# Kernel optimization log

Measured on AMD Instinct MI355X. Metric: run time of the kernel, lower is better.

## Reference

```python
import jax, jax.numpy as jnp
import numpy as np

N = 100000   # nodes
E = 1600000  # edges (avg degree 16)
D = 128      # in = hidden = out channels
DROP_P = 0.2


def setup_inputs() -> dict:
    key = jax.random.key(0)
    ks = jax.random.split(key, 11)
    s = 1.0 / np.sqrt(D)  # glorot-ish scale
    inp = {
        "features": jax.random.normal(ks[0], (N, D), jnp.float32),
        "edge_index": jax.random.randint(ks[1], (2, E), 0, N, dtype=jnp.int64),
    }
    for i in range(3):
        inp[f"Wl{i}"] = jax.random.normal(ks[2 + 3 * i], (D, D), jnp.float32) * s
        inp[f"Wr{i}"] = jax.random.normal(ks[3 + 3 * i], (D, D), jnp.float32) * s
        inp[f"b{i}"] = jnp.zeros((D,), jnp.float32)
    return inp


def _sage_conv(x, src, dst, Wl, Wr, b):
    # PyG SAGEConv (aggr='max'): out = lin_l(max_{j->i} x_j) + lin_r(x_i)
    agg = jax.ops.segment_max(x[src], dst, num_segments=N)  # [N, D_in]
    agg = jnp.where(jnp.isfinite(agg), agg, 0.0)  # isolated nodes -> 0 (torch_scatter zero-init)
    return agg @ Wl + x @ Wr + b


def _dropout(x, key, p=DROP_P):
    keep = jax.random.bernoulli(key, 1.0 - p, x.shape)
    return jnp.where(keep, x / (1.0 - p), 0.0)


def reference(features, edge_index, Wl0, Wr0, b0, Wl1, Wr1, b1, Wl2, Wr2, b2):
    src, dst = edge_index[0], edge_index[1]
    k1, k2 = jax.random.split(jax.random.key(42))
    x = _sage_conv(features, src, dst, Wl0, Wr0, b0)
    x = _dropout(jax.nn.elu(x), k1)
    x = _sage_conv(x, src, dst, Wl1, Wr1, b1)
    x = _dropout(jax.nn.elu(x), k2)
    x = _sage_conv(x, src, dst, Wl2, Wr2, b2)
    return x
```

## Files before the change

kernel.cpp:

```cpp
#include <hip/hip_runtime.h>
#include <math.h>

#define D 128
#define CHUNK 1024
#define BSHIFT 9
#define BCAP 12288

typedef __attribute__((ext_vector_type(8))) _Float16 half8;
typedef __attribute__((ext_vector_type(4))) float floatx4;

__host__ __device__ __forceinline__ unsigned rotl32(unsigned v, int r) {
  return (v << r) | (v >> (32 - r));
}

__host__ __device__ __forceinline__ void threefry2x32(unsigned k0, unsigned k1,
                                                      unsigned x0, unsigned x1,
                                                      unsigned &o0, unsigned &o1) {
  unsigned ks2 = k0 ^ k1 ^ 0x1BD11BDAu;
  unsigned v0 = x0 + k0;
  unsigned v1 = x1 + k1;
  v0 += v1; v1 = rotl32(v1, 13); v1 ^= v0;
  v0 += v1; v1 = rotl32(v1, 15); v1 ^= v0;
  v0 += v1; v1 = rotl32(v1, 26); v1 ^= v0;
  v0 += v1; v1 = rotl32(v1, 6);  v1 ^= v0;
  v0 += k1; v1 += ks2 + 1u;
  v0 += v1; v1 = rotl32(v1, 17); v1 ^= v0;
  v0 += v1; v1 = rotl32(v1, 29); v1 ^= v0;
  v0 += v1; v1 = rotl32(v1, 16); v1 ^= v0;
  v0 += v1; v1 = rotl32(v1, 24); v1 ^= v0;
  v0 += ks2; v1 += k0 + 2u;
  v0 += v1; v1 = rotl32(v1, 13); v1 ^= v0;
  v0 += v1; v1 = rotl32(v1, 15); v1 ^= v0;
  v0 += v1; v1 = rotl32(v1, 26); v1 ^= v0;
  v0 += v1; v1 = rotl32(v1, 6);  v1 ^= v0;
  v0 += k0; v1 += k1 + 3u;
  v0 += v1; v1 = rotl32(v1, 17); v1 ^= v0;
  v0 += v1; v1 = rotl32(v1, 29); v1 ^= v0;
  v0 += v1; v1 = rotl32(v1, 16); v1 ^= v0;
  v0 += v1; v1 = rotl32(v1, 24); v1 ^= v0;
  v0 += k1; v1 += ks2 + 4u;
  v0 += v1; v1 = rotl32(v1, 13); v1 ^= v0;
  v0 += v1; v1 = rotl32(v1, 15); v1 ^= v0;
  v0 += v1; v1 = rotl32(v1, 26); v1 ^= v0;
  v0 += v1; v1 = rotl32(v1, 6);  v1 ^= v0;
  v0 += ks2; v1 += k0 + 5u;
  o0 = v0; o1 = v1;
}

__device__ __forceinline__ unsigned short f2h(float f) {
  _Float16 h = (_Float16)f;
  return *(unsigned short*)&h;
}

__device__ __forceinline__ unsigned pkmax(unsigned a, unsigned b) {
  unsigned r;
  asm("v_pk_max_f16 %0, %1, %2" : "=v"(r) : "v"(a), "v"(b));
  return r;
}

__global__ __launch_bounds__(256) void hist_kernel(
    const int* __restrict__ dst, int* __restrict__ counts, int nEdges) {
  int e = blockIdx.x * 256 + threadIdx.x;
  if (e < nEdges) atomicAdd(&counts[dst[e]], 1);
}

__global__ __launch_bounds__(256) void reduce_chunk_kernel(
    const int* __restrict__ counts, int* __restrict__ blockSums, int nNodes) {
  __shared__ int s[256];
  int t = threadIdx.x;
  int base = blockIdx.x * CHUNK + t * 4;
  int sum = 0;
#pragma unroll
  for (int i = 0; i < 4; ++i)
    if (base + i < nNodes) sum += counts[base + i];
  s[t] = sum;
  __syncthreads();
  for (int off = 128; off > 0; off >>= 1) {
    if (t < off) s[t] += s[t + off];
    __syncthreads();
  }
  if (t == 0) blockSums[blockIdx.x] = s[0];
}

__global__ void scan_block_sums_kernel(int* blockSums, int nChunks) {
  if (threadIdx.x == 0 && blockIdx.x == 0) {
    int run = 0;
    for (int i = 0; i < nChunks; ++i) {
      int v = blockSums[i];
      blockSums[i] = run;
      run += v;
    }
    blockSums[nChunks] = run;
  }
}

__global__ __launch_bounds__(256) void scan_chunk_kernel(
    const int* __restrict__ counts, const int* __restrict__ blockOffs,
    int* __restrict__ rowStart, int* __restrict__ cursor, int nNodes) {
  __shared__ int sSum[256];
  int t = threadIdx.x;
  int base = blockIdx.x * CHUNK + t * 4;
  int c0 = 0, c1 = 0, c2 = 0, c3 = 0;
  if (base + 0 < nNodes) c0 = counts[base + 0];
  if (base + 1 < nNodes) c1 = counts[base + 1];
  if (base + 2 < nNodes) c2 = counts[base + 2];
  if (base + 3 < nNodes) c3 = counts[base + 3];
  int local = c0 + c1 + c2 + c3;
  sSum[t] = local;
  __syncthreads();
  for (int off = 1; off < 256; off <<= 1) {
    int v = (t >= off) ? sSum[t - off] : 0;
    __syncthreads();
    sSum[t] += v;
    __syncthreads();
  }
  int excl = blockOffs[blockIdx.x] + sSum[t] - local;
  int p0 = excl, p1 = p0 + c0, p2 = p1 + c1, p3 = p2 + c2;
  if (base + 0 < nNodes) { rowStart[base + 0] = p0; cursor[base + 0] = p0;
                           if (base + 0 == nNodes - 1) rowStart[nNodes] = p1; }
  if (base + 1 < nNodes) { rowStart[base + 1] = p1; cursor[base + 1] = p1;
                           if (base + 1 == nNodes - 1) rowStart[nNodes] = p2; }
  if (base + 2 < nNodes) { rowStart[base + 2] = p2; cursor[base + 2] = p2;
                           if (base + 2 == nNodes - 1) rowStart[nNodes] = p3; }
  if (base + 3 < nNodes) { rowStart[base + 3] = p3; cursor[base + 3] = p3;
                           if (base + 3 == nNodes - 1) rowStart[nNodes] = p3 + c3; }
}

__global__ void init_bucket_cursor_kernel(
    const int* __restrict__ rowStart, int* __restrict__ bucketCursor,
    int nBuck, int nNodes) {
  int b = blockIdx.x * 256 + threadIdx.x;
  if (b <= nBuck) {
    int n = b << BSHIFT;
    if (n > nNodes) n = nNodes;
    bucketCursor[b] = rowStart[n];
  }
}

__global__ __launch_bounds__(256) void bucket_scatter_kernel(
    const int* __restrict__ src, const int* __restrict__ dst,
    int* __restrict__ bucketCursor, uint2* __restrict__ pairs,
    int nEdges, int nBuck) {
  __shared__ int lcount[256];
  __shared__ int lbase[256];
  __shared__ int loff[256];
  int t = threadIdx.x;
  lcount[t] = 0; loff[t] = 0;
  __syncthreads();
  int e0 = blockIdx.x * 4096;
  for (int i = t; i < 4096; i += 256) {
    int e = e0 + i;
    if (e < nEdges) atomicAdd(&lcount[dst[e] >> BSHIFT], 1);
  }
  __syncthreads();
  if (t < nBuck) {
    int c = lcount[t];
    if (c > 0) lbase[t] = atomicAdd(&bucketCursor[t], c);
  }
  __syncthreads();
  for (int i = t; i < 4096; i += 256) {
    int e = e0 + i;
    if (e < nEdges) {
      int d = dst[e];
      int b = d >> BSHIFT;
      int lp = atomicAdd(&loff[b], 1);
      pairs[lbase[b] + lp] = make_uint2((unsigned)src[e], (unsigned)d);
    }
  }
}

__global__ __launch_bounds__(256) void local_fill_kernel(
    const uint2* __restrict__ pairs, const int* __restrict__ rowStart,
    int* __restrict__ cursor, int* __restrict__ csrSrc, int nNodes) {
  __shared__ int sData[BCAP];
  __shared__ int lcur[1 << BSHIFT];
  int b = blockIdx.x;
  int node0 = b << BSHIFT;
  int node1 = node0 + (1 << BSHIFT);
  if (node1 > nNodes) node1 = nNodes;
  int base = rowStart[node0];
  int end = rowStart[node1];
  int cnt = end - base;
  int t = threadIdx.x;
  for (int i = t; i < node1 - node0; i += 256)
    lcur[i] = rowStart[node0 + i] - base;
  __syncthreads();
  if (cnt <= BCAP) {
    for (int i = base + t; i < end; i += 256) {
      uint2 p = pairs[i];
      int lp = atomicAdd(&lcur[p.y - (unsigned)node0], 1);
      sData[lp] = (int)p.x;
    }
    __syncthreads();
    for (int i = t; i < cnt; i += 256)
      csrSrc[base + i] = sData[i];
  } else {
    for (int i = base + t; i < end; i += 256) {
      uint2 p = pairs[i];
      int pos = atomicAdd(&cursor[p.y], 1);
      csrSrc[pos] = (int)p.x;
    }
  }
}

__global__ __launch_bounds__(256) void convert_feat_kernel(
    const float* __restrict__ f, unsigned short* __restrict__ o, int nElems) {
  int i = (blockIdx.x * 256 + threadIdx.x) * 4;
  if (i + 3 < nElems) {
    float4 v = *((const float4*)(f + i));
    unsigned a = (unsigned)f2h(v.x) | ((unsigned)f2h(v.y) << 16);
    unsigned b = (unsigned)f2h(v.z) | ((unsigned)f2h(v.w) << 16);
    *((uint2*)(o + i)) = make_uint2(a, b);
  } else {
    for (int j = i; j < nElems; ++j) o[j] = f2h(f[j]);
  }
}

__global__ __launch_bounds__(256) void pack_weights_kernel(
    const float* __restrict__ Wl0, const float* __restrict__ Wr0,
    const float* __restrict__ Wl1, const float* __restrict__ Wr1,
    const float* __restrict__ Wl2, const float* __restrict__ Wr2,
    unsigned short* __restrict__ Wt) {
  int t = blockIdx.x * 256 + threadIdx.x;
  if (t >= 3 * 128 * 256) return;
  int l = t >> 15;
  int rem = t & 32767;
  int n = rem >> 8;
  int k = rem & 255;
  const float* Wl = (l == 0) ? Wl0 : (l == 1) ? Wl1 : Wl2;
  const float* Wr = (l == 0) ? Wr0 : (l == 1) ? Wr1 : Wr2;
  float v = (k < 128) ? Wl[k * D + n] : Wr[(k - 128) * D + n];
  Wt[t] = f2h(v);
}

__global__ __launch_bounds__(256) void gather_max_f16_kernel(
    const uint4* __restrict__ x8, const int* __restrict__ rowStart,
    const int* __restrict__ csrSrc, uint4* __restrict__ agg8, int nNodes) {
  int n = blockIdx.x * 4 + (threadIdx.x >> 6);
  if (n >= nNodes) return;
  int lane = threadIdx.x & 63;
  int q = lane >> 4;
  int l16 = lane & 15;
  int e0 = rowStart[n], e1 = rowStart[n + 1];
  unsigned m0 = 0xFC00FC00u, m1 = 0xFC00FC00u,
           m2 = 0xFC00FC00u, m3 = 0xFC00FC00u;
  int e = e0;
  for (; e + 7 < e1; e += 8) {
    int sa = csrSrc[e + q];
    int sb = csrSrc[e + 4 + q];
    uint4 va = x8[(size_t)sa * 16 + l16];
    uint4 vb = x8[(size_t)sb * 16 + l16];
    m0 = pkmax(m0, pkmax(va.x, vb.x));
    m1 = pkmax(m1, pkmax(va.y, vb.y));
    m2 = pkmax(m2, pkmax(va.z, vb.z));
    m3 = pkmax(m3, pkmax(va.w, vb.w));
  }
  if (e + 3 < e1) {
    int sa = csrSrc[e + q];
    uint4 va = x8[(size_t)sa * 16 + l16];
    m0 = pkmax(m0, va.x); m1 = pkmax(m1, va.y);
    m2 = pkmax(m2, va.z); m3 = pkmax(m3, va.w);
    e += 4;
  }
  for (; e < e1; ++e) {
    int sa = csrSrc[e];
    uint4 va = x8[(size_t)sa * 16 + l16];
    m0 = pkmax(m0, va.x); m1 = pkmax(m1, va.y);
    m2 = pkmax(m2, va.z); m3 = pkmax(m3, va.w);
  }
  m0 = pkmax(m0, (unsigned)__shfl_xor((int)m0, 16, 64));
  m1 = pkmax(m1, (unsigned)__shfl_xor((int)m1, 16, 64));
  m2 = pkmax(m2, (unsigned)__shfl_xor((int)m2, 16, 64));
  m3 = pkmax(m3, (unsigned)__shfl_xor((int)m3, 16, 64));
  m0 = pkmax(m0, (unsigned)__shfl_xor((int)m0, 32, 64));
  m1 = pkmax(m1, (unsigned)__shfl_xor((int)m1, 32, 64));
  m2 = pkmax(m2, (unsigned)__shfl_xor((int)m2, 32, 64));
  m3 = pkmax(m3, (unsigned)__shfl_xor((int)m3, 32, 64));
  uint4 r = make_uint4(0u, 0u, 0u, 0u);
  if (e0 != e1) r = make_uint4(m0, m1, m2, m3);
  if (q == 0) agg8[(size_t)n * 16 + l16] = r;
}

#define PA 280

__global__ __launch_bounds__(256) void fused_mfma_kernel(
    const unsigned short* __restrict__ agghf, unsigned short* __restrict__ xhf,
    const unsigned short* __restrict__ Wt, const float* __restrict__ bias,
    float* __restrict__ outF, int nRows, int mode, unsigned kk0, unsigned kk1) {
  __shared__ unsigned short sA[32 * PA];

  const int tid = threadIdx.x;
  const int row0 = blockIdx.x * 32;
  const int wv = tid >> 6, lane = tid & 63;
  const int quad = lane >> 4, m16 = lane & 15;
  const int nbase = wv * 32;

#pragma unroll
  for (int i = 0; i < 4; ++i) {
    int idx = i * 256 + tid;
    int r = idx >> 5;
    int seg = idx & 31;
    uint4 v = make_uint4(0, 0, 0, 0);
    if (row0 + r < nRows) {
      if (seg < 16) v = ((const uint4*)(agghf + (size_t)(row0 + r) * D))[seg];
      else          v = ((const uint4*)(xhf  + (size_t)(row0 + r) * D))[seg - 16];
    }
    *((uint4*)(sA + r * PA + seg * 8)) = v;
  }

  half8 bfr[2][4][2];
#pragma unroll
  for (int kc = 0; kc < 2; ++kc)
#pragma unroll
    for (int ks = 0; ks < 4; ++ks)
#pragma unroll
      for (int j = 0; j < 2; ++j)
        bfr[kc][ks][j] = *((const half8*)(
            Wt + (size_t)(nbase + j * 16 + m16) * 256 + kc * 128 + ks * 32 + quad * 8));

  floatx4 acc[2][2];
#pragma unroll
  for (int i = 0; i < 2; ++i)
#pragma unroll
    for (int j = 0; j < 2; ++j) acc[i][j] = (floatx4)(0.0f);

  __syncthreads();

#pragma unroll
  for (int kc = 0; kc < 2; ++kc)
#pragma unroll
    for (int ks = 0; ks < 4; ++ks) {
      int kA = kc * 128 + ks * 32 + quad * 8;
      half8 a0 = *((const half8*)(sA + m16 * PA + kA));
      half8 a1 = *((const half8*)(sA + (m16 + 16) * PA + kA));
      acc[0][0] = __builtin_amdgcn_mfma_f32_16x16x32_f16(a0, bfr[kc][ks][0], acc[0][0], 0, 0, 0);
      acc[0][1] = __builtin_amdgcn_mfma_f32_16x16x32_f16(a0, bfr[kc][ks][1], acc[0][1], 0, 0, 0);
      acc[1][0] = __builtin_amdgcn_mfma_f32_16x16x32_f16(a1, bfr[kc][ks][0], acc[1][0], 0, 0, 0);
      acc[1][1] = __builtin_amdgcn_mfma_f32_16x16x32_f16(a1, bfr[kc][ks][1], acc[1][1], 0, 0, 0);
    }

#pragma unroll
  for (int j = 0; j < 2; ++j) {
    int col = nbase + j * 16 + m16;
    float bc = bias[col];
#pragma unroll
    for (int i = 0; i < 2; ++i) {
#pragma unroll
      for (int reg = 0; reg < 4; ++reg) {
        int r = row0 + i * 16 + quad * 4 + reg;
        if (r >= nRows) continue;
        float v = acc[i][j][reg] + bc;
        if (mode < 2) {
          v = (v > 0.0f) ? v : expm1f(v);
          unsigned jj = (unsigned)r * D + col;
          unsigned y0, y1;
          threefry2x32(kk0, kk1, 0u, jj, y0, y1);
          float u = __uint_as_float((((y0 ^ y1) >> 9)) | 0x3F800000u) - 1.0f;
          v = (u < 0.8f) ? v * 1.25f : 0.0f;
          xhf[(size_t)r * D + col] = f2h(v);
        } else {
          outF[(size_t)r * D + col] = v;
        }
      }
    }
  }
}

extern "C" void kernel_launch(void* const* d_in, const int* in_sizes, int n_in,
                              void* d_out, int out_size, void* d_ws, size_t ws_size,
                              hipStream_t stream) {
  const float* feat = (const float*)d_in[0];
  const int* ei = (const int*)d_in[1];
  const float* Wl0 = (const float*)d_in[2];
  const float* Wr0 = (const float*)d_in[3];
  const float* b0 = (const float*)d_in[4];
  const float* Wl1 = (const float*)d_in[5];
  const float* Wr1 = (const float*)d_in[6];
  const float* b1 = (const float*)d_in[7];
  const float* Wl2 = (const float*)d_in[8];
  const float* Wr2 = (const float*)d_in[9];
  const float* b2 = (const float*)d_in[10];

  const int N = in_sizes[0] / D;
  const int E = in_sizes[1] / 2;
  const int* src = ei;
  const int* dst = ei + E;

  const size_t hfBytes = (size_t)N * D * 2;
  char* wsp = (char*)d_ws;
  size_t off = 0;
  unsigned short* xhf   = (unsigned short*)(wsp + off); off += hfBytes;
  unsigned short* agghf = (unsigned short*)(wsp + off); off += hfBytes;
  unsigned short* Wt    = (unsigned short*)(wsp + off); off += ((size_t)3 * 128 * 256 * 2 + 511) & ~511ull;
  int* rowStart  = (int*)(wsp + off); off += ((size_t)(N + 1) * 4 + 511) & ~511ull;
  int* cursor    = (int*)(wsp + off); off += ((size_t)N * 4 + 511) & ~511ull;
  int* blockSums = (int*)(wsp + off); off += 2048;
  int* bucketCursor = (int*)(wsp + off); off += 4096;
  int* csrSrc    = (int*)(wsp + off); off += (size_t)E * 4;
  uint2* pairs   = (uint2*)(wsp + off); off += (size_t)E * 8;

  const int nChunks = (N + CHUNK - 1) / CHUNK;
  const int nBuck = (N + (1 << BSHIFT) - 1) >> BSHIFT;

  unsigned k1a, k1b, k2a, k2b;
  threefry2x32(0u, 42u, 0u, 0u, k1a, k1b);
  threefry2x32(0u, 42u, 0u, 1u, k2a, k2b);

  hipMemsetAsync(cursor, 0, (size_t)N * 4, stream);
  hist_kernel<<<(E + 255) / 256, 256, 0, stream>>>(dst, cursor, E);
  reduce_chunk_kernel<<<nChunks, 256, 0, stream>>>(cursor, blockSums, N);
  scan_block_sums_kernel<<<1, 64, 0, stream>>>(blockSums, nChunks);
  scan_chunk_kernel<<<nChunks, 256, 0, stream>>>(cursor, blockSums, rowStart, cursor, N);
  init_bucket_cursor_kernel<<<(nBuck + 256) / 256, 256, 0, stream>>>(rowStart, bucketCursor, nBuck, N);
  bucket_scatter_kernel<<<(E + 4095) / 4096, 256, 0, stream>>>(src, dst, bucketCursor, pairs, E, nBuck);
  local_fill_kernel<<<nBuck, 256, 0, stream>>>(pairs, rowStart, cursor, csrSrc, N);

  convert_feat_kernel<<<(N * D / 4 + 255) / 256, 256, 0, stream>>>(feat, xhf, N * D);
  pack_weights_kernel<<<(3 * 128 * 256 + 255) / 256, 256, 0, stream>>>(
      Wl0, Wr0, Wl1, Wr1, Wl2, Wr2, Wt);

  dim3 blk(256);
  dim3 grdMax((N + 3) / 4);
  dim3 grdGemm((N + 31) / 32);
  float* outF = (float*)d_out;

  gather_max_f16_kernel<<<grdMax, blk, 0, stream>>>((const uint4*)xhf, rowStart, csrSrc, (uint4*)agghf, N);
  fused_mfma_kernel<<<grdGemm, blk, 0, stream>>>(agghf, xhf, Wt, b0, outF, N, 0, k1a, k1b);

  gather_max_f16_kernel<<<grdMax, blk, 0, stream>>>((const uint4*)xhf, rowStart, csrSrc, (uint4*)agghf, N);
  fused_mfma_kernel<<<grdGemm, blk, 0, stream>>>(agghf, xhf, Wt + 32768, b1, outF, N, 1, k2a, k2b);

  gather_max_f16_kernel<<<grdMax, blk, 0, stream>>>((const uint4*)xhf, rowStart, csrSrc, (uint4*)agghf, N);
  fused_mfma_kernel<<<grdGemm, blk, 0, stream>>>(agghf, xhf, Wt + 65536, b2, outF, N, 2, 0u, 0u);
}
```

Before: 588.9 us.

## Build CSR via bucket-level counts and pack edge pairs into one word

Replaces the per-node global histogram and the multi-kernel prefix scan with a per-bucket count, a single-block bucket scan, and a per-node count and scan done in shared memory inside local_fill_kernel, which also writes rowStart. Edge pairs are packed into 32 bits (source shifted left by 9 bits, low 9 bits of the destination) instead of uint2, halving the scratch traffic. This removes several launches and the global atomics on 100k counters. The packing only works while source ids fit in 23 bits and there are at most 256 buckets.

```diff
diff --git a/kernel.cpp b/kernel.cpp
--- a/kernel.cpp
+++ b/kernel.cpp
@@ -2,7 +2,6 @@
 #include <math.h>
 
 #define D 128
-#define CHUNK 1024
 #define BSHIFT 9
 #define BCAP 12288
 
@@ -58,88 +57,49 @@
   return r;
 }
 
-__global__ __launch_bounds__(256) void hist_kernel(
-    const int* __restrict__ dst, int* __restrict__ counts, int nEdges) {
-  int e = blockIdx.x * 256 + threadIdx.x;
-  if (e < nEdges) atomicAdd(&counts[dst[e]], 1);
-}
-
-__global__ __launch_bounds__(256) void reduce_chunk_kernel(
-    const int* __restrict__ counts, int* __restrict__ blockSums, int nNodes) {
+
+__global__ __launch_bounds__(256) void bucket_count_kernel(
+    const int* __restrict__ dst, int* __restrict__ bucketTotal, int nEdges) {
+  __shared__ int lc[256];
+  int t = threadIdx.x;
+  lc[t] = 0;
+  __syncthreads();
+  int e0 = blockIdx.x * 4096;
+  for (int i = t; i < 4096; i += 256) {
+    int e = e0 + i;
+    if (e < nEdges) atomicAdd(&lc[dst[e] >> BSHIFT], 1);
+  }
+  __syncthreads();
+  int c = lc[t];
+  if (c > 0) atomicAdd(&bucketTotal[t], c);
+}
+
+__global__ __launch_bounds__(256) void scan_buckets_kernel(
+    const int* __restrict__ bucketTotal, int* __restrict__ buckOff,
+    int* __restrict__ bucketCursor, int nBuck) {
   __shared__ int s[256];
   int t = threadIdx.x;
-  int base = blockIdx.x * CHUNK + t * 4;
-  int sum = 0;
-#pragma unroll
-  for (int i = 0; i < 4; ++i)
-    if (base + i < nNodes) sum += counts[base + i];
-  s[t] = sum;
-  __syncthreads();
-  for (int off = 128; off > 0; off >>= 1) {
-    if (t < off) s[t] += s[t + off];
+  int v = (t < nBuck) ? bucketTotal[t] : 0;
+  s[t] = v;
+  __syncthreads();
+  for (int off = 1; off < 256; off <<= 1) {
+    int u = (t >= off) ? s[t - off] : 0;
     __syncthreads();
-  }
-  if (t == 0) blockSums[blockIdx.x] = s[0];
-}
-
-__global__ void scan_block_sums_kernel(int* blockSums, int nChunks) {
-  if (threadIdx.x == 0 && blockIdx.x == 0) {
-    int run = 0;
-    for (int i = 0; i < nChunks; ++i) {
-      int v = blockSums[i];
-      blockSums[i] = run;
-      run += v;
-    }
-    blockSums[nChunks] = run;
-  }
-}
-
-__global__ __launch_bounds__(256) void scan_chunk_kernel(
-    const int* __restrict__ counts, const int* __restrict__ blockOffs,
-    int* __restrict__ rowStart, int* __restrict__ cursor, int nNodes) {
-  __shared__ int sSum[256];
-  int t = threadIdx.x;
-  int base = blockIdx.x * CHUNK + t * 4;
-  int c0 = 0, c1 = 0, c2 = 0, c3 = 0;
-  if (base + 0 < nNodes) c0 = counts[base + 0];
-  if (base + 1 < nNodes) c1 = counts[base + 1];
-  if (base + 2 < nNodes) c2 = counts[base + 2];
-  if (base + 3 < nNodes) c3 = counts[base + 3];
-  int local = c0 + c1 + c2 + c3;
-  sSum[t] = local;
-  __syncthreads();
-  for (int off = 1; off < 256; off <<= 1) {
-    int v = (t >= off) ? sSum[t - off] : 0;
+    s[t] += u;
     __syncthreads();
-    sSum[t] += v;
-    __syncthreads();
-  }
-  int excl = blockOffs[blockIdx.x] + sSum[t] - local;
-  int p0 = excl, p1 = p0 + c0, p2 = p1 + c1, p3 = p2 + c2;
-  if (base + 0 < nNodes) { rowStart[base + 0] = p0; cursor[base + 0] = p0;
-                           if (base + 0 == nNodes - 1) rowStart[nNodes] = p1; }
-  if (base + 1 < nNodes) { rowStart[base + 1] = p1; cursor[base + 1] = p1;
-                           if (base + 1 == nNodes - 1) rowStart[nNodes] = p2; }
-  if (base + 2 < nNodes) { rowStart[base + 2] = p2; cursor[base + 2] = p2;
-                           if (base + 2 == nNodes - 1) rowStart[nNodes] = p3; }
-  if (base + 3 < nNodes) { rowStart[base + 3] = p3; cursor[base + 3] = p3;
-                           if (base + 3 == nNodes - 1) rowStart[nNodes] = p3 + c3; }
-}
-
-__global__ void init_bucket_cursor_kernel(
-    const int* __restrict__ rowStart, int* __restrict__ bucketCursor,
-    int nBuck, int nNodes) {
-  int b = blockIdx.x * 256 + threadIdx.x;
-  if (b <= nBuck) {
-    int n = b << BSHIFT;
-    if (n > nNodes) n = nNodes;
-    bucketCursor[b] = rowStart[n];
+  }
+  int excl = s[t] - v;
+  if (t < nBuck) {
+    buckOff[t] = excl;
+    bucketCursor[t] = excl;
+  } else if (t == nBuck) {
+    buckOff[t] = s[255];
   }
 }
 
 __global__ __launch_bounds__(256) void bucket_scatter_kernel(
     const int* __restrict__ src, const int* __restrict__ dst,
-    int* __restrict__ bucketCursor, uint2* __restrict__ pairs,
+    int* __restrict__ bucketCursor, unsigned* __restrict__ pairs,
     int nEdges, int nBuck) {
   __shared__ int lcount[256];
   __shared__ int lbase[256];
@@ -164,41 +124,69 @@
       int d = dst[e];
       int b = d >> BSHIFT;
       int lp = atomicAdd(&loff[b], 1);
-      pairs[lbase[b] + lp] = make_uint2((unsigned)src[e], (unsigned)d);
+      pairs[lbase[b] + lp] = ((unsigned)src[e] << BSHIFT) | ((unsigned)d & 511u);
     }
   }
 }
 
 __global__ __launch_bounds__(256) void local_fill_kernel(
-    const uint2* __restrict__ pairs, const int* __restrict__ rowStart,
-    int* __restrict__ cursor, int* __restrict__ csrSrc, int nNodes) {
+    const unsigned* __restrict__ pairs, const int* __restrict__ buckOff,
+    int* __restrict__ rowStart, int* __restrict__ csrSrc,
+    int nNodes, int nBuck) {
   __shared__ int sData[BCAP];
-  __shared__ int lcur[1 << BSHIFT];
+  __shared__ int lcnt[1 << BSHIFT];
+  __shared__ int sSum[256];
   int b = blockIdx.x;
   int node0 = b << BSHIFT;
-  int node1 = node0 + (1 << BSHIFT);
-  if (node1 > nNodes) node1 = nNodes;
-  int base = rowStart[node0];
-  int end = rowStart[node1];
+  int base = buckOff[b];
+  int end = buckOff[b + 1];
   int cnt = end - base;
   int t = threadIdx.x;
-  for (int i = t; i < node1 - node0; i += 256)
-    lcur[i] = rowStart[node0 + i] - base;
-  __syncthreads();
+
+  lcnt[t] = 0;
+  lcnt[t + 256] = 0;
+  __syncthreads();
+
+  for (int i = base + t; i < end; i += 256)
+    atomicAdd(&lcnt[pairs[i] & 511u], 1);
+  __syncthreads();
+
+  int c0 = lcnt[2 * t];
+  int c1 = lcnt[2 * t + 1];
+  int local = c0 + c1;
+  sSum[t] = local;
+  __syncthreads();
+  for (int off = 1; off < 256; off <<= 1) {
+    int v = (t >= off) ? sSum[t - off] : 0;
+    __syncthreads();
+    sSum[t] += v;
+    __syncthreads();
+  }
+  int excl = sSum[t] - local;
+  __syncthreads();
+  lcnt[2 * t] = excl;
+  lcnt[2 * t + 1] = excl + c0;
+  int n0 = node0 + 2 * t;
+  int n1 = n0 + 1;
+  if (n0 < nNodes) rowStart[n0] = base + excl;
+  if (n1 < nNodes) rowStart[n1] = base + excl + c0;
+  if (b == nBuck - 1 && t == 255) rowStart[nNodes] = end;
+  __syncthreads();
+
   if (cnt <= BCAP) {
     for (int i = base + t; i < end; i += 256) {
-      uint2 p = pairs[i];
-      int lp = atomicAdd(&lcur[p.y - (unsigned)node0], 1);
-      sData[lp] = (int)p.x;
+      unsigned p = pairs[i];
+      int lp = atomicAdd(&lcnt[p & 511u], 1);
+      sData[lp] = (int)(p >> BSHIFT);
     }
     __syncthreads();
     for (int i = t; i < cnt; i += 256)
       csrSrc[base + i] = sData[i];
   } else {
     for (int i = base + t; i < end; i += 256) {
-      uint2 p = pairs[i];
-      int pos = atomicAdd(&cursor[p.y], 1);
-      csrSrc[pos] = (int)p.x;
+      unsigned p = pairs[i];
+      int lp = atomicAdd(&lcnt[p & 511u], 1);
+      csrSrc[base + lp] = (int)(p >> BSHIFT);
     }
   }
 }
@@ -392,28 +380,24 @@
   unsigned short* xhf   = (unsigned short*)(wsp + off); off += hfBytes;
   unsigned short* agghf = (unsigned short*)(wsp + off); off += hfBytes;
   unsigned short* Wt    = (unsigned short*)(wsp + off); off += ((size_t)3 * 128 * 256 * 2 + 511) & ~511ull;
-  int* rowStart  = (int*)(wsp + off); off += ((size_t)(N + 1) * 4 + 511) & ~511ull;
-  int* cursor    = (int*)(wsp + off); off += ((size_t)N * 4 + 511) & ~511ull;
-  int* blockSums = (int*)(wsp + off); off += 2048;
-  int* bucketCursor = (int*)(wsp + off); off += 4096;
+  int* rowStart     = (int*)(wsp + off); off += ((size_t)(N + 1) * 4 + 511) & ~511ull;
+  int* bucketTotal  = (int*)(wsp + off); off += 2048;
+  int* buckOff      = (int*)(wsp + off); off += 2048;
+  int* bucketCursor = (int*)(wsp + off); off += 2048;
   int* csrSrc    = (int*)(wsp + off); off += (size_t)E * 4;
-  uint2* pairs   = (uint2*)(wsp + off); off += (size_t)E * 8;
-
-  const int nChunks = (N + CHUNK - 1) / CHUNK;
+  unsigned* pairs = (unsigned*)(wsp + off); off += (size_t)E * 4;
+
   const int nBuck = (N + (1 << BSHIFT) - 1) >> BSHIFT;
 
   unsigned k1a, k1b, k2a, k2b;
   threefry2x32(0u, 42u, 0u, 0u, k1a, k1b);
   threefry2x32(0u, 42u, 0u, 1u, k2a, k2b);
 
-  hipMemsetAsync(cursor, 0, (size_t)N * 4, stream);
-  hist_kernel<<<(E + 255) / 256, 256, 0, stream>>>(dst, cursor, E);
-  reduce_chunk_kernel<<<nChunks, 256, 0, stream>>>(cursor, blockSums, N);
-  scan_block_sums_kernel<<<1, 64, 0, stream>>>(blockSums, nChunks);
-  scan_chunk_kernel<<<nChunks, 256, 0, stream>>>(cursor, blockSums, rowStart, cursor, N);
-  init_bucket_cursor_kernel<<<(nBuck + 256) / 256, 256, 0, stream>>>(rowStart, bucketCursor, nBuck, N);
+  hipMemsetAsync(bucketTotal, 0, 1024, stream);
+  bucket_count_kernel<<<(E + 4095) / 4096, 256, 0, stream>>>(dst, bucketTotal, E);
+  scan_buckets_kernel<<<1, 256, 0, stream>>>(bucketTotal, buckOff, bucketCursor, nBuck);
   bucket_scatter_kernel<<<(E + 4095) / 4096, 256, 0, stream>>>(src, dst, bucketCursor, pairs, E, nBuck);
-  local_fill_kernel<<<nBuck, 256, 0, stream>>>(pairs, rowStart, cursor, csrSrc, N);
+  local_fill_kernel<<<nBuck, 256, 0, stream>>>(pairs, buckOff, rowStart, csrSrc, N, nBuck);
 
   convert_feat_kernel<<<(N * D / 4 + 255) / 256, 256, 0, stream>>>(feat, xhf, N * D);
   pack_weights_kernel<<<(3 * 128 * 256 + 255) / 256, 256, 0, stream>>>(
```

After: 521.9 us. 11.4% less time.
